# Kernel optimization log

Hardware: AMD Instinct MI355X
Metric: run time of the kernel (lower is better)

## Reference

```python
import jax, jax.numpy as jnp
import numpy as np

B, S, D = 8, 512, 512
H, DK = 64, 8          # 64 heads hardcoded in SelfAttentiveLBLBiLM
WIDTH = 16             # local window width
NL = 2                 # highway layers
N = S + 2 * WIDTH      # padded sequence length


def setup_inputs() -> dict:
    key = jax.random.key(0)
    ks = jax.random.split(key, 12)
    s = 0.02
    return {
        "inputs": jax.random.normal(ks[0], (B, S, D), jnp.float32),
        "left_pad": jax.random.normal(ks[1], (WIDTH, D), jnp.float32) * s,
        "right_pad": jax.random.normal(ks[2], (WIDTH, D), jnp.float32) * s,
        "l_Wqkv": jax.random.normal(ks[3], (3, D, D), jnp.float32) * s,
        "l_bqkv": jnp.zeros((3, D), jnp.float32),
        "l_Wo": jax.random.normal(ks[4], (D, D), jnp.float32) * s,
        "l_bo": jnp.zeros((D,), jnp.float32),
        "r_Wqkv": jax.random.normal(ks[5], (3, D, D), jnp.float32) * s,
        "r_bqkv": jnp.zeros((3, D), jnp.float32),
        "r_Wo": jax.random.normal(ks[6], (D, D), jnp.float32) * s,
        "r_bo": jnp.zeros((D,), jnp.float32),
        "lhw_W": jax.random.normal(ks[7], (NL, 2 * D, D), jnp.float32) * s,
        "lhw_b": jnp.zeros((NL, 2 * D), jnp.float32),
        "rhw_W": jax.random.normal(ks[8], (NL, 2 * D, D), jnp.float32) * s,
        "rhw_b": jnp.zeros((NL, 2 * D), jnp.float32),
    }


def _masks(n, width):
    i = jnp.arange(n)[:, None]
    j = jnp.arange(n)[None, :]
    # local_mask: triu(k=-width-1) * (1 - triu(k=1)) -> i-width-1 <= j <= i
    left = (j <= i) & (j >= i - width - 1)
    # right mask is the full flip of the left mask
    right = (j >= i) & (j <= i + width + 1)
    return left, right


def _mha(x, Wqkv, bqkv, Wo, bo, mask):
    b, n, d = x.shape
    # torch Linear: y = x @ W.T + b, W is [out, in]
    qkv = jnp.einsum("bnd,tod->tbno", x, Wqkv) + bqkv[:, None, None, :]
    q, k, v = [t.reshape(b, n, H, DK).transpose(0, 2, 1, 3) for t in qkv]
    scores = jnp.einsum("bhqd,bhkd->bhqk", q, k) / jnp.sqrt(jnp.float32(DK))
    scores = jnp.where(mask[None, None], scores, jnp.float32(-1e9))
    p = jax.nn.softmax(scores, axis=-1)
    out = jnp.einsum("bhqk,bhkd->bhqd", p, v)
    out = out.transpose(0, 2, 1, 3).reshape(b, n, d)
    return out @ Wo.T + bo


def _highway(x, Ws, bs):
    for l in range(NL):
        proj = x @ Ws[l].T + bs[l]
        nonlin = jax.nn.relu(proj[..., :D])
        gate = jax.nn.sigmoid(proj[..., D:])
        x = gate * x + (1.0 - gate) * nonlin
    return x


def reference(inputs, left_pad, right_pad, l_Wqkv, l_bqkv, l_Wo, l_bo,
              r_Wqkv, r_bqkv, r_Wo, r_bo, lhw_W, lhw_b, rhw_W, rhw_b):
    b = inputs.shape[0]
    new_inputs = jnp.concatenate(
        [jnp.broadcast_to(left_pad[None], (b, WIDTH, D)), inputs,
         jnp.broadcast_to(right_pad[None], (b, WIDTH, D))], axis=1)  # [B, N, D]
    left_mask, right_mask = _masks(N, WIDTH)
    new_left = _mha(new_inputs, l_Wqkv, l_bqkv, l_Wo, l_bo, left_mask)
    new_right = _mha(new_inputs, r_Wqkv, r_bqkv, r_Wo, r_bo, right_mask)
    # per-step loop indexes position start + width -> slice [WIDTH : WIDTH + S]
    left_out = _highway(new_left[:, WIDTH:WIDTH + S], lhw_W, lhw_b)
    right_out = _highway(new_right[:, WIDTH:WIDTH + S], rhw_W, rhw_b)
    last = jnp.concatenate([left_out, right_out], axis=-1)  # [B, S, 2D]
    all_layers = last[None]  # [1, B, S, 2D] (single layer stacked on dim 0)
    return (all_layers, last)
```

## Files before the change

### kernel.cpp

```cpp
#include <hip/hip_runtime.h>
#include <math.h>

#define B_ 8
#define S_ 512
#define D_ 512
#define WIDTH_ 16
#define NSEQ 544
#define MROWS 4352
#define MOUT 4096
#define OUTHALF 4194304

typedef _Float16 half8 __attribute__((ext_vector_type(8)));
typedef _Float16 half4 __attribute__((ext_vector_type(4)));
typedef _Float16 half2_t __attribute__((ext_vector_type(2)));
typedef float floatx4 __attribute__((ext_vector_type(4)));

#if defined(__has_builtin)
#if __has_builtin(__builtin_amdgcn_fdot2)
#define HAS_FDOT2 1
#endif
#endif

#define GLD16(g, l) __builtin_amdgcn_global_load_lds(                          \
    (const __attribute__((address_space(1))) void*)(g),                        \
    (__attribute__((address_space(3))) void*)(l), 16, 0, 0)

#define WAIT_VM(n)  asm volatile("s_waitcnt vmcnt(" #n ")" ::: "memory")
#define WAIT_LGKM0() asm volatile("s_waitcnt lgkmcnt(0)" ::: "memory")
#define BARRIER()                                                              \
    do {                                                                       \
        __builtin_amdgcn_s_barrier();                                          \
        asm volatile("" ::: "memory");                                         \
    } while (0)

__device__ __forceinline__ float sigmoidf_(float x) {
    return 1.f / (1.f + __expf(-x));
}

__global__ __launch_bounds__(256)
void gemm_qkv(const _Float16* __restrict__ A,
              const _Float16* __restrict__ B0, const _Float16* __restrict__ B1,
              const float* __restrict__ bias0, const float* __restrict__ bias1,
              _Float16* __restrict__ C16) {
    const int lda = 512, ldb = 512, ldc = 1536;
    __shared__ _Float16 As[2][128 * 32];
    __shared__ _Float16 Bs[2][128 * 32];
    const int t    = threadIdx.x;
    const int wave = t >> 6;
    const int lane = t & 63;
    const int bm = blockIdx.y * 128;
    const int bn = blockIdx.x * 128;
    const int z  = blockIdx.z;
    const _Float16* B = z ? B1 : B0;
    const float* bias = z ? bias1 : bias0;
    _Float16* C = C16 + (size_t)z * MROWS * 1536;
    const int wm = (wave & 1) * 64;
    const int wn = (wave >> 1) * 64;

    const int inst = wave * 2;
    const int r0 = inst * 16 + (lane >> 2);
    const int kf = (lane & 3) * 8;

    const _Float16* Ag0 = A + (size_t)(bm + r0) * lda + kf;
    const _Float16* Ag1 = Ag0 + (size_t)16 * lda;
    const _Float16* Bg0 = B + (size_t)(bn + r0) * ldb + kf;
    const _Float16* Bg1 = Bg0 + (size_t)16 * ldb;
    const int so = inst * 512;

    const int fr = lane & 15;
    const int fq = (lane >> 4) * 8;

    floatx4 acc[4][4] = {};

#define QKV_STAGE(bf_, koff_)                                                  \
    do {                                                                       \
        GLD16(Ag0 + (koff_), &As[bf_][so]);                                    \
        GLD16(Ag1 + (koff_), &As[bf_][so + 512]);                              \
        GLD16(Bg0 + (koff_), &Bs[bf_][so]);                                    \
        GLD16(Bg1 + (koff_), &Bs[bf_][so + 512]);                              \
    } while (0)

    QKV_STAGE(0, 0);
    QKV_STAGE(1, 32);

#pragma unroll
    for (int tt = 0; tt < 16; tt++) {
        const int c = tt & 1;
        if (tt == 15) WAIT_VM(0);
        else          WAIT_VM(4);
        BARRIER();
        half8 af[4], bf[4];
#pragma unroll
        for (int s = 0; s < 4; s++) {
            af[s] = *(const half8*)&As[c][(wm + s * 16 + fr) * 32 + fq];
            bf[s] = *(const half8*)&Bs[c][(wn + s * 16 + fr) * 32 + fq];
        }
        WAIT_LGKM0();
        BARRIER();
        if (tt + 2 < 16) QKV_STAGE(c, (tt + 2) * 32);
#pragma unroll
        for (int i = 0; i < 4; i++)
#pragma unroll
            for (int j = 0; j < 4; j++)
                acc[i][j] = __builtin_amdgcn_mfma_f32_16x16x32_f16(
                    af[i], bf[j], acc[i][j], 0, 0, 0);
    }
#undef QKV_STAGE

    const int rq = (lane >> 4) * 4;
    const int cc = lane & 15;
#pragma unroll
    for (int i = 0; i < 4; i++) {
        const int rbase = bm + wm + i * 16 + rq;
#pragma unroll
        for (int j = 0; j < 4; j++) {
            const int col = bn + wn + j * 16 + cc;
            const float bv = bias[col];
#pragma unroll
            for (int r = 0; r < 4; r++)
                C[(size_t)(rbase + r) * ldc + col] = (_Float16)(acc[i][j][r] + bv);
        }
    }
}

__global__ __launch_bounds__(256)
void gemm_wo(const _Float16* __restrict__ Aall,
             const _Float16* __restrict__ B0, const _Float16* __restrict__ B1,
             const float* __restrict__ bias0, const float* __restrict__ bias1,
             _Float16* __restrict__ x16base) {
    const int lda = 512, ldb = 512;
    __shared__ _Float16 As[2][64 * 32];
    __shared__ _Float16 Bs[2][128 * 32];
    const int t    = threadIdx.x;
    const int wave = t >> 6;
    const int lane = t & 63;
    const int bm = blockIdx.y * 64;
    const int bn = blockIdx.x * 128;
    const int z  = blockIdx.z;
    const _Float16* A = Aall + (size_t)z * MROWS * 512;
    const _Float16* B = z ? B1 : B0;
    const float* bias = z ? bias1 : bias0;
    _Float16* x16 = x16base + (size_t)z * MOUT * 512;

    const int wm = (wave & 1) * 32;
    const int wn = (wave >> 1) * 64;

    const int rA = wave * 16 + (lane >> 2);
    const int rB = wave * 32 + (lane >> 2);
    const int kf = (lane & 3) * 8;

    const _Float16* Ag0 = A + (size_t)(bm + rA) * lda + kf;
    const _Float16* Bg0 = B + (size_t)(bn + rB) * ldb + kf;
    const _Float16* Bg1 = Bg0 + (size_t)16 * ldb;
    const int soA = wave * 512;
    const int soB = wave * 1024;

    const int fr = lane & 15;
    const int fq = (lane >> 4) * 8;

    floatx4 acc[2][4] = {};

#define WO_STAGE(bf_, koff_)                                                   \
    do {                                                                       \
        GLD16(Ag0 + (koff_), &As[bf_][soA]);                                   \
        GLD16(Bg0 + (koff_), &Bs[bf_][soB]);                                   \
        GLD16(Bg1 + (koff_), &Bs[bf_][soB + 512]);                             \
    } while (0)

    WO_STAGE(0, 0);
    WO_STAGE(1, 32);

#pragma unroll
    for (int tt = 0; tt < 16; tt++) {
        const int c = tt & 1;
        if (tt == 15) WAIT_VM(0);
        else          WAIT_VM(3);
        BARRIER();
        half8 af[2], bf[4];
#pragma unroll
        for (int s = 0; s < 2; s++)
            af[s] = *(const half8*)&As[c][(wm + s * 16 + fr) * 32 + fq];
#pragma unroll
        for (int s = 0; s < 4; s++)
            bf[s] = *(const half8*)&Bs[c][(wn + s * 16 + fr) * 32 + fq];
        WAIT_LGKM0();
        BARRIER();
        if (tt + 2 < 16) WO_STAGE(c, (tt + 2) * 32);
#pragma unroll
        for (int i = 0; i < 2; i++)
#pragma unroll
            for (int j = 0; j < 4; j++)
                acc[i][j] = __builtin_amdgcn_mfma_f32_16x16x32_f16(
                    af[i], bf[j], acc[i][j], 0, 0, 0);
    }
#undef WO_STAGE

    const int rq = (lane >> 4) * 4;
    const int cc = lane & 15;
#pragma unroll
    for (int i = 0; i < 2; i++) {
        const int rbase = bm + wm + i * 16 + rq;
#pragma unroll
        for (int r = 0; r < 4; r++) {
            const int row = rbase + r;
            const int b = row / NSEQ;
            const int s = row - b * NSEQ;
            if (s < WIDTH_ || s >= WIDTH_ + S_) continue;
            const int m = b * S_ + s - WIDTH_;
#pragma unroll
            for (int j = 0; j < 4; j++) {
                const int col = bn + wn + j * 16 + cc;
                x16[(size_t)m * 512 + col] = (_Float16)(acc[i][j][r] + bias[col]);
            }
        }
    }
}

__global__ __launch_bounds__(256)
void gemm_hw(const _Float16* __restrict__ x16inbase,
             const _Float16* __restrict__ W0, const _Float16* __restrict__ W1,
             const float* __restrict__ b0, const float* __restrict__ b1,
             _Float16* __restrict__ x16outbase,
             float* __restrict__ outlastbase,
             float* __restrict__ outallbase) {
    const int lda = 512, ldb = 512;
    __shared__ _Float16 As[2][128 * 32];
    __shared__ _Float16 Bn[2][64 * 32];
    __shared__ _Float16 Bg[2][64 * 32];
    const int t    = threadIdx.x;
    const int wave = t >> 6;
    const int lane = t & 63;
    const int bm = blockIdx.y * 128;
    const int bn = blockIdx.x * 64;
    const int z  = blockIdx.z;
    const _Float16* A = x16inbase + (size_t)z * MOUT * 512;
    const _Float16* W = z ? W1 : W0;
    const float* bias = z ? b1 : b0;
    _Float16* x16out = x16outbase ? x16outbase + (size_t)z * MOUT * 512 : nullptr;

    const int wm = (wave & 1) * 64;
    const int wn = (wave >> 1) * 32;

    const int rA = wave * 32 + (lane >> 2);
    const int rB = wave * 16 + (lane >> 2);
    const int kf = (lane & 3) * 8;

    const _Float16* Ag0 = A + (size_t)(bm + rA) * lda + kf;
    const _Float16* Ag1 = Ag0 + (size_t)16 * lda;
    const _Float16* Bn0 = W + (size_t)(bn + rB) * ldb + kf;
    const _Float16* Bg0 = W + (size_t)(512 + bn + rB) * ldb + kf;
    const int soA = wave * 1024;
    const int soB = wave * 512;

    const int fr = lane & 15;
    const int fq = (lane >> 4) * 8;

    floatx4 accn[4][2] = {};
    floatx4 accg[4][2] = {};

#define HW_STAGE(bf_, koff_)                                                   \
    do {                                                                       \
        GLD16(Ag0 + (koff_), &As[bf_][soA]);                                   \
        GLD16(Ag1 + (koff_), &As[bf_][soA + 512]);                             \
        GLD16(Bn0 + (koff_), &Bn[bf_][soB]);                                   \
        GLD16(Bg0 + (koff_), &Bg[bf_][soB]);                                   \
    } while (0)

    HW_STAGE(0, 0);
    HW_STAGE(1, 32);

#pragma unroll
    for (int tt = 0; tt < 16; tt++) {
        const int c = tt & 1;
        if (tt == 15) WAIT_VM(0);
        else          WAIT_VM(4);
        BARRIER();
        half8 af[4], bnf[2], bgf[2];
#pragma unroll
        for (int s = 0; s < 4; s++)
            af[s] = *(const half8*)&As[c][(wm + s * 16 + fr) * 32 + fq];
#pragma unroll
        for (int s = 0; s < 2; s++) {
            bnf[s] = *(const half8*)&Bn[c][(wn + s * 16 + fr) * 32 + fq];
            bgf[s] = *(const half8*)&Bg[c][(wn + s * 16 + fr) * 32 + fq];
        }
        WAIT_LGKM0();
        BARRIER();
        if (tt + 2 < 16) HW_STAGE(c, (tt + 2) * 32);
#pragma unroll
        for (int i = 0; i < 4; i++)
#pragma unroll
            for (int j = 0; j < 2; j++) {
                accn[i][j] = __builtin_amdgcn_mfma_f32_16x16x32_f16(
                    af[i], bnf[j], accn[i][j], 0, 0, 0);
                accg[i][j] = __builtin_amdgcn_mfma_f32_16x16x32_f16(
                    af[i], bgf[j], accg[i][j], 0, 0, 0);
            }
    }
#undef HW_STAGE

    float* outlast = outlastbase ? outlastbase + z * 512 : nullptr;
    float* outall  = outallbase  ? outallbase  + z * 512 : nullptr;

    const int rq = (lane >> 4) * 4;
    const int cc = lane & 15;
#pragma unroll
    for (int i = 0; i < 4; i++) {
        const int rbase = bm + wm + i * 16 + rq;
#pragma unroll
        for (int j = 0; j < 2; j++) {
            const int col = bn + wn + j * 16 + cc;
            const float bnl = bias[col];
            const float bgt = bias[512 + col];
#pragma unroll
            for (int r = 0; r < 4; r++) {
                const int row = rbase + r;
                const float nl = fmaxf(accn[i][j][r] + bnl, 0.f);
                const float g  = sigmoidf_(accg[i][j][r] + bgt);
                const float xo = (float)A[(size_t)row * 512 + col];
                const float v  = g * xo + (1.f - g) * nl;
                if (x16out) {
                    x16out[(size_t)row * 512 + col] = (_Float16)v;
                } else {
                    outlast[(size_t)row * 1024 + col] = v;
                    outall[(size_t)row * 1024 + col] = v;
                }
            }
        }
    }
}

__global__ __launch_bounds__(256)
void attn_win(const _Float16* __restrict__ qkvall, _Float16* __restrict__ attall) {
    const int dir = blockIdx.y;
    const int dlo = dir ? 0 : -(WIDTH_ + 1);
    const _Float16* qkv = qkvall + (size_t)dir * MROWS * 1536;
    _Float16* att = attall + (size_t)dir * MROWS * 512;
    const int tid = blockIdx.x * 256 + threadIdx.x;
    const int h  = tid & 63;
    const int bi = tid >> 6;
    const int i  = bi % NSEQ;
    const int b  = bi / NSEQ;
    const int j0 = i + dlo;
    const float scale = 0.35355339059327373f;

    const half8 q8 = *(const half8*)(qkv + (size_t)bi * 1536 + h * 8);
#if !defined(HAS_FDOT2)
    float q[8];
#pragma unroll
    for (int d = 0; d < 8; d++) q[d] = (float)q8[d];
#endif

    float s[18];
    float mx = -1e30f;
#pragma unroll
    for (int jj = 0; jj < 18; jj++) {
        const int j = j0 + jj;
        const int jc = j < 0 ? 0 : (j > NSEQ - 1 ? NSEQ - 1 : j);
        const half8 k8 = *(const half8*)(qkv + (size_t)(b * NSEQ + jc) * 1536 + 512 + h * 8);
        float d = 0.f;
#if defined(HAS_FDOT2)
#pragma unroll
        for (int p = 0; p < 4; p++) {
            half2_t qa = { q8[2 * p], q8[2 * p + 1] };
            half2_t ka = { k8[2 * p], k8[2 * p + 1] };
            d = __builtin_amdgcn_fdot2(qa, ka, d, false);
        }
#else
#pragma unroll
        for (int dd = 0; dd < 8; dd++) d = fmaf(q[dd], (float)k8[dd], d);
#endif
        s[jj] = (j == jc) ? d * scale : -1e30f;
        mx = fmaxf(mx, s[jj]);
    }
    float sum = 0.f;
#pragma unroll
    for (int jj = 0; jj < 18; jj++) { s[jj] = __expf(s[jj] - mx); sum += s[jj]; }
    const float inv = 1.f / sum;

    float o[8] = {};
#pragma unroll
    for (int jj = 0; jj < 18; jj++) {
        const int j = j0 + jj;
        const int jc = j < 0 ? 0 : (j > NSEQ - 1 ? NSEQ - 1 : j);
        const half8 v8 = *(const half8*)(qkv + (size_t)(b * NSEQ + jc) * 1536 + 1024 + h * 8);
        const float p = s[jj];
#pragma unroll
        for (int dd = 0; dd < 8; dd++) o[dd] = fmaf(p, (float)v8[dd], o[dd]);
    }
    half8 o16;
#pragma unroll
    for (int d = 0; d < 8; d++) o16[d] = (_Float16)(o[d] * inv);
    *(half8*)&att[(size_t)bi * 512 + h * 8] = o16;
}

__global__ void prep(const float* __restrict__ lq, const float* __restrict__ rq,
                     const float* __restrict__ lo, const float* __restrict__ ro,
                     const float* __restrict__ lh, const float* __restrict__ rh,
                     _Float16* __restrict__ wdst,
                     const float* __restrict__ inp,
                     const float* __restrict__ lp,
                     const float* __restrict__ rp,
                     _Float16* __restrict__ padX) {
    const int gb = blockIdx.x;
    if (gb < 4096) {
        int idx = gb * 256 + threadIdx.x;
        const float* src; int off;
        if      (idx < 196608) { src = lq; off = idx; }
        else if (idx < 393216) { src = rq; off = idx - 196608; }
        else if (idx < 458752) { src = lo; off = idx - 393216; }
        else if (idx < 524288) { src = ro; off = idx - 458752; }
        else if (idx < 786432) { src = lh; off = idx - 524288; }
        else                   { src = rh; off = idx - 786432; }
        const float4 v = ((const float4*)src)[off];
        half4 h = { (_Float16)v.x, (_Float16)v.y, (_Float16)v.z, (_Float16)v.w };
        ((half4*)wdst)[idx] = h;
    } else {
        int idx = (gb - 4096) * 256 + threadIdx.x;
        const int c4 = idx & 127;
        const int t  = idx >> 7;
        const int n = t % NSEQ;
        const int b = t / NSEQ;
        const float* src;
        if (n < WIDTH_)            src = lp + n * 512;
        else if (n < WIDTH_ + S_)  src = inp + ((size_t)(b * S_ + n - WIDTH_)) * 512;
        else                       src = rp + (n - WIDTH_ - S_) * 512;
        const float4 v = *(const float4*)(src + c4 * 4);
        half4 h = { (_Float16)v.x, (_Float16)v.y, (_Float16)v.z, (_Float16)v.w };
        *(half4*)&padX[(size_t)t * 512 + c4 * 4] = h;
    }
}

extern "C" void kernel_launch(void* const* d_in, const int* in_sizes, int n_in,
                              void* d_out, int out_size, void* d_ws, size_t ws_size,
                              hipStream_t stream) {
    const float* inputs    = (const float*)d_in[0];
    const float* left_pad  = (const float*)d_in[1];
    const float* right_pad = (const float*)d_in[2];
    const float* l_Wqkv = (const float*)d_in[3];
    const float* l_bqkv = (const float*)d_in[4];
    const float* l_Wo   = (const float*)d_in[5];
    const float* l_bo   = (const float*)d_in[6];
    const float* r_Wqkv = (const float*)d_in[7];
    const float* r_bqkv = (const float*)d_in[8];
    const float* r_Wo   = (const float*)d_in[9];
    const float* r_bo   = (const float*)d_in[10];
    const float* lhw_W  = (const float*)d_in[11];
    const float* lhw_b  = (const float*)d_in[12];
    const float* rhw_W  = (const float*)d_in[13];
    const float* rhw_b  = (const float*)d_in[14];

    float* out = (float*)d_out;
    _Float16* h = (_Float16*)d_ws;

    _Float16* padX16 = h;
    _Float16* w16    = h + 2228224;
    _Float16* lqkv16 = w16;
    _Float16* rqkv16 = w16 + 786432;
    _Float16* lWo16  = w16 + 1572864;
    _Float16* rWo16  = w16 + 1835008;
    _Float16* lhw16  = w16 + 2097152;
    _Float16* rhw16  = w16 + 3145728;
    _Float16* qkv16  = h + 6422528;
    _Float16* att16  = h + 19791872;
    _Float16* x16a   = h + 24248320;
    _Float16* x16b   = h + 28442624;

    float* out_all  = out;
    float* out_last = out + OUTHALF;

    prep<<<6272, 256, 0, stream>>>(l_Wqkv, r_Wqkv, l_Wo, r_Wo, lhw_W, rhw_W, w16,
                                   inputs, left_pad, right_pad, padX16);

    gemm_qkv<<<dim3(12, 34, 2), 256, 0, stream>>>(
        padX16, lqkv16, rqkv16, l_bqkv, r_bqkv, qkv16);

    attn_win<<<dim3(MROWS * 64 / 256, 2), 256, 0, stream>>>(qkv16, att16);

    gemm_wo<<<dim3(4, 68, 2), 256, 0, stream>>>(
        att16, lWo16, rWo16, l_bo, r_bo, x16a);

    gemm_hw<<<dim3(8, 32, 2), 256, 0, stream>>>(
        x16a, lhw16, rhw16, lhw_b, rhw_b, x16b, nullptr, nullptr);
    gemm_hw<<<dim3(8, 32, 2), 256, 0, stream>>>(
        x16b, lhw16 + 524288, rhw16 + 524288, lhw_b + 1024, rhw_b + 1024,
        nullptr, out_last, out_all);
}
```

Measured before the change: 217.2 us.

## Add XCD block swizzle, LDS-staged epilogues, and multi-query attention reuse

Adds an XCD-aware block index remap to the three GEMMs so neighbouring tiles land on the same L2. The QKV and first highway GEMM epilogues now go through LDS and write 16-byte coalesced rows instead of scattered 2-byte stores. The windowed attention kernel has each thread handle 4 consecutive queries, loading each K/V row once and sharing it across them. It also drops the max-subtraction in the softmax, which risks overflow with large scores and changes launch parallelism to 544 blocks.

After: 185.4 us (median of 2 runs). -14.6%, faster.

```diff
diff --git a/kernel.cpp b/kernel.cpp
--- a/kernel.cpp
+++ b/kernel.cpp
@@ -12,14 +12,7 @@
 
 typedef _Float16 half8 __attribute__((ext_vector_type(8)));
 typedef _Float16 half4 __attribute__((ext_vector_type(4)));
-typedef _Float16 half2_t __attribute__((ext_vector_type(2)));
 typedef float floatx4 __attribute__((ext_vector_type(4)));
-
-#if defined(__has_builtin)
-#if __has_builtin(__builtin_amdgcn_fdot2)
-#define HAS_FDOT2 1
-#endif
-#endif
 
 #define GLD16(g, l) __builtin_amdgcn_global_load_lds(                          \
     (const __attribute__((address_space(1))) void*)(g),                        \
@@ -37,20 +30,32 @@
     return 1.f / (1.f + __expf(-x));
 }
 
+__device__ __forceinline__ void xcd_swz(const int nx, const int ny,
+                                        int& bx, int& by, int& bz) {
+    const int flat = blockIdx.x + nx * (blockIdx.y + ny * blockIdx.z);
+    const int nwg  = nx * ny * 2;
+    const int t2   = (flat & 7) * (nwg >> 3) + (flat >> 3);
+    bz = t2 / (nx * ny);
+    const int rem = t2 - bz * nx * ny;
+    by = rem / nx;
+    bx = rem - by * nx;
+}
+
 __global__ __launch_bounds__(256)
 void gemm_qkv(const _Float16* __restrict__ A,
               const _Float16* __restrict__ B0, const _Float16* __restrict__ B1,
               const float* __restrict__ bias0, const float* __restrict__ bias1,
               _Float16* __restrict__ C16) {
     const int lda = 512, ldb = 512, ldc = 1536;
-    __shared__ _Float16 As[2][128 * 32];
-    __shared__ _Float16 Bs[2][128 * 32];
+    __shared__ _Float16 SH[16384];
+    int bx, by, bz;
+    xcd_swz(12, 34, bx, by, bz);
     const int t    = threadIdx.x;
     const int wave = t >> 6;
     const int lane = t & 63;
-    const int bm = blockIdx.y * 128;
-    const int bn = blockIdx.x * 128;
-    const int z  = blockIdx.z;
+    const int bm = by * 128;
+    const int bn = bx * 128;
+    const int z  = bz;
     const _Float16* B = z ? B1 : B0;
     const float* bias = z ? bias1 : bias0;
     _Float16* C = C16 + (size_t)z * MROWS * 1536;
@@ -74,10 +79,10 @@
 
 #define QKV_STAGE(bf_, koff_)                                                  \
     do {                                                                       \
-        GLD16(Ag0 + (koff_), &As[bf_][so]);                                    \
-        GLD16(Ag1 + (koff_), &As[bf_][so + 512]);                              \
-        GLD16(Bg0 + (koff_), &Bs[bf_][so]);                                    \
-        GLD16(Bg1 + (koff_), &Bs[bf_][so + 512]);                              \
+        GLD16(Ag0 + (koff_), &SH[(bf_) * 4096 + so]);                          \
+        GLD16(Ag1 + (koff_), &SH[(bf_) * 4096 + so + 512]);                    \
+        GLD16(Bg0 + (koff_), &SH[8192 + (bf_) * 4096 + so]);                   \
+        GLD16(Bg1 + (koff_), &SH[8192 + (bf_) * 4096 + so + 512]);             \
     } while (0)
 
     QKV_STAGE(0, 0);
@@ -92,8 +97,8 @@
         half8 af[4], bf[4];
 #pragma unroll
         for (int s = 0; s < 4; s++) {
-            af[s] = *(const half8*)&As[c][(wm + s * 16 + fr) * 32 + fq];
-            bf[s] = *(const half8*)&Bs[c][(wn + s * 16 + fr) * 32 + fq];
+            af[s] = *(const half8*)&SH[c * 4096 + (wm + s * 16 + fr) * 32 + fq];
+            bf[s] = *(const half8*)&SH[8192 + c * 4096 + (wn + s * 16 + fr) * 32 + fq];
         }
         WAIT_LGKM0();
         BARRIER();
@@ -111,15 +116,25 @@
     const int cc = lane & 15;
 #pragma unroll
     for (int i = 0; i < 4; i++) {
-        const int rbase = bm + wm + i * 16 + rq;
 #pragma unroll
         for (int j = 0; j < 4; j++) {
-            const int col = bn + wn + j * 16 + cc;
-            const float bv = bias[col];
+            const int col = wn + j * 16 + cc;
+            const float bv = bias[bn + col];
 #pragma unroll
             for (int r = 0; r < 4; r++)
-                C[(size_t)(rbase + r) * ldc + col] = (_Float16)(acc[i][j][r] + bv);
-        }
+                SH[(wm + i * 16 + rq + r) * 128 + col] =
+                    (_Float16)(acc[i][j][r] + bv);
+        }
+    }
+    WAIT_LGKM0();
+    BARRIER();
+#pragma unroll
+    for (int it = 0; it < 8; it++) {
+        const int flat = it * 256 + t;
+        const int row = flat >> 4;
+        const int ch  = flat & 15;
+        *(half8*)&C[(size_t)(bm + row) * ldc + bn + ch * 8] =
+            *(const half8*)&SH[row * 128 + ch * 8];
     }
 }
 
@@ -131,12 +146,14 @@
     const int lda = 512, ldb = 512;
     __shared__ _Float16 As[2][64 * 32];
     __shared__ _Float16 Bs[2][128 * 32];
+    int bx, by, bz;
+    xcd_swz(4, 68, bx, by, bz);
     const int t    = threadIdx.x;
     const int wave = t >> 6;
     const int lane = t & 63;
-    const int bm = blockIdx.y * 64;
-    const int bn = blockIdx.x * 128;
-    const int z  = blockIdx.z;
+    const int bm = by * 64;
+    const int bn = bx * 128;
+    const int z  = bz;
     const _Float16* A = Aall + (size_t)z * MROWS * 512;
     const _Float16* B = z ? B1 : B0;
     const float* bias = z ? bias1 : bias0;
@@ -224,15 +241,17 @@
              float* __restrict__ outlastbase,
              float* __restrict__ outallbase) {
     const int lda = 512, ldb = 512;
-    __shared__ _Float16 As[2][128 * 32];
+    __shared__ _Float16 SA[8192];
     __shared__ _Float16 Bn[2][64 * 32];
     __shared__ _Float16 Bg[2][64 * 32];
+    int bx, by, bz;
+    xcd_swz(8, 32, bx, by, bz);
     const int t    = threadIdx.x;
     const int wave = t >> 6;
     const int lane = t & 63;
-    const int bm = blockIdx.y * 128;
-    const int bn = blockIdx.x * 64;
-    const int z  = blockIdx.z;
+    const int bm = by * 128;
+    const int bn = bx * 64;
+    const int z  = bz;
     const _Float16* A = x16inbase + (size_t)z * MOUT * 512;
     const _Float16* W = z ? W1 : W0;
     const float* bias = z ? b1 : b0;
@@ -260,8 +279,8 @@
 
 #define HW_STAGE(bf_, koff_)                                                   \
     do {                                                                       \
-        GLD16(Ag0 + (koff_), &As[bf_][soA]);                                   \
-        GLD16(Ag1 + (koff_), &As[bf_][soA + 512]);                             \
+        GLD16(Ag0 + (koff_), &SA[(bf_) * 4096 + soA]);                         \
+        GLD16(Ag1 + (koff_), &SA[(bf_) * 4096 + soA + 512]);                   \
         GLD16(Bn0 + (koff_), &Bn[bf_][soB]);                                   \
         GLD16(Bg0 + (koff_), &Bg[bf_][soB]);                                   \
     } while (0)
@@ -278,7 +297,7 @@
         half8 af[4], bnf[2], bgf[2];
 #pragma unroll
         for (int s = 0; s < 4; s++)
-            af[s] = *(const half8*)&As[c][(wm + s * 16 + fr) * 32 + fq];
+            af[s] = *(const half8*)&SA[c * 4096 + (wm + s * 16 + fr) * 32 + fq];
 #pragma unroll
         for (int s = 0; s < 2; s++) {
             bnf[s] = *(const half8*)&Bn[c][(wn + s * 16 + fr) * 32 + fq];
@@ -299,29 +318,54 @@
     }
 #undef HW_STAGE
 
-    float* outlast = outlastbase ? outlastbase + z * 512 : nullptr;
-    float* outall  = outallbase  ? outallbase  + z * 512 : nullptr;
-
     const int rq = (lane >> 4) * 4;
     const int cc = lane & 15;
-#pragma unroll
-    for (int i = 0; i < 4; i++) {
-        const int rbase = bm + wm + i * 16 + rq;
-#pragma unroll
-        for (int j = 0; j < 2; j++) {
-            const int col = bn + wn + j * 16 + cc;
-            const float bnl = bias[col];
-            const float bgt = bias[512 + col];
-#pragma unroll
-            for (int r = 0; r < 4; r++) {
-                const int row = rbase + r;
-                const float nl = fmaxf(accn[i][j][r] + bnl, 0.f);
-                const float g  = sigmoidf_(accg[i][j][r] + bgt);
-                const float xo = (float)A[(size_t)row * 512 + col];
-                const float v  = g * xo + (1.f - g) * nl;
-                if (x16out) {
-                    x16out[(size_t)row * 512 + col] = (_Float16)v;
-                } else {
+    if (x16out) {
+#pragma unroll
+        for (int i = 0; i < 4; i++) {
+#pragma unroll
+            for (int j = 0; j < 2; j++) {
+                const int col = wn + j * 16 + cc;
+                const float bnl = bias[bn + col];
+                const float bgt = bias[512 + bn + col];
+#pragma unroll
+                for (int r = 0; r < 4; r++) {
+                    const int row = wm + i * 16 + rq + r;
+                    const float nl = fmaxf(accn[i][j][r] + bnl, 0.f);
+                    const float g  = sigmoidf_(accg[i][j][r] + bgt);
+                    const float xo = (float)A[(size_t)(bm + row) * 512 + bn + col];
+                    SA[row * 64 + col] = (_Float16)(g * xo + (1.f - g) * nl);
+                }
+            }
+        }
+        WAIT_LGKM0();
+        BARRIER();
+#pragma unroll
+        for (int it = 0; it < 4; it++) {
+            const int flat = it * 256 + t;
+            const int row = flat >> 3;
+            const int ch  = flat & 7;
+            *(half8*)&x16out[(size_t)(bm + row) * 512 + bn + ch * 8] =
+                *(const half8*)&SA[row * 64 + ch * 8];
+        }
+    } else {
+        float* outlast = outlastbase + z * 512;
+        float* outall  = outallbase  + z * 512;
+#pragma unroll
+        for (int i = 0; i < 4; i++) {
+            const int rbase = bm + wm + i * 16 + rq;
+#pragma unroll
+            for (int j = 0; j < 2; j++) {
+                const int col = bn + wn + j * 16 + cc;
+                const float bnl = bias[col];
+                const float bgt = bias[512 + col];
+#pragma unroll
+                for (int r = 0; r < 4; r++) {
+                    const int row = rbase + r;
+                    const float nl = fmaxf(accn[i][j][r] + bnl, 0.f);
+                    const float g  = sigmoidf_(accg[i][j][r] + bgt);
+                    const float xo = (float)A[(size_t)row * 512 + col];
+                    const float v  = g * xo + (1.f - g) * nl;
                     outlast[(size_t)row * 1024 + col] = v;
                     outall[(size_t)row * 1024 + col] = v;
                 }
@@ -332,66 +376,64 @@
 
 __global__ __launch_bounds__(256)
 void attn_win(const _Float16* __restrict__ qkvall, _Float16* __restrict__ attall) {
-    const int dir = blockIdx.y;
-    const int dlo = dir ? 0 : -(WIDTH_ + 1);
+    const int sb  = (blockIdx.x & 7) * 68 + (blockIdx.x >> 3);
+    const int wid = threadIdx.x >> 6;
+    const int h   = threadIdx.x & 63;
+    const int wflat = sb * 4 + wid;
+    const int ig  = wflat % 136;
+    const int db  = wflat / 136;
+    const int b   = db & 7;
+    const int dir = db >> 3;
+    const int i0  = ig * 4;
+    const int dlo = dir ? 0 : -17;
     const _Float16* qkv = qkvall + (size_t)dir * MROWS * 1536;
     _Float16* att = attall + (size_t)dir * MROWS * 512;
-    const int tid = blockIdx.x * 256 + threadIdx.x;
-    const int h  = tid & 63;
-    const int bi = tid >> 6;
-    const int i  = bi % NSEQ;
-    const int b  = bi / NSEQ;
-    const int j0 = i + dlo;
+    const size_t rowb = (size_t)b * NSEQ;
     const float scale = 0.35355339059327373f;
 
-    const half8 q8 = *(const half8*)(qkv + (size_t)bi * 1536 + h * 8);
-#if !defined(HAS_FDOT2)
-    float q[8];
-#pragma unroll
-    for (int d = 0; d < 8; d++) q[d] = (float)q8[d];
-#endif
-
-    float s[18];
-    float mx = -1e30f;
-#pragma unroll
-    for (int jj = 0; jj < 18; jj++) {
+    float q[4][8];
+#pragma unroll
+    for (int tq = 0; tq < 4; tq++) {
+        const half8 q8 = *(const half8*)(qkv + (rowb + i0 + tq) * 1536 + h * 8);
+#pragma unroll
+        for (int d = 0; d < 8; d++) q[tq][d] = (float)q8[d];
+    }
+
+    float o[4][8] = {};
+    float sum[4] = {};
+    const int j0 = i0 + dlo;
+
+#pragma unroll
+    for (int jj = 0; jj < 21; jj++) {
         const int j = j0 + jj;
-        const int jc = j < 0 ? 0 : (j > NSEQ - 1 ? NSEQ - 1 : j);
-        const half8 k8 = *(const half8*)(qkv + (size_t)(b * NSEQ + jc) * 1536 + 512 + h * 8);
-        float d = 0.f;
-#if defined(HAS_FDOT2)
-#pragma unroll
-        for (int p = 0; p < 4; p++) {
-            half2_t qa = { q8[2 * p], q8[2 * p + 1] };
-            half2_t ka = { k8[2 * p], k8[2 * p + 1] };
-            d = __builtin_amdgcn_fdot2(qa, ka, d, false);
-        }
-#else
-#pragma unroll
-        for (int dd = 0; dd < 8; dd++) d = fmaf(q[dd], (float)k8[dd], d);
-#endif
-        s[jj] = (j == jc) ? d * scale : -1e30f;
-        mx = fmaxf(mx, s[jj]);
-    }
-    float sum = 0.f;
-#pragma unroll
-    for (int jj = 0; jj < 18; jj++) { s[jj] = __expf(s[jj] - mx); sum += s[jj]; }
-    const float inv = 1.f / sum;
-
-    float o[8] = {};
-#pragma unroll
-    for (int jj = 0; jj < 18; jj++) {
-        const int j = j0 + jj;
-        const int jc = j < 0 ? 0 : (j > NSEQ - 1 ? NSEQ - 1 : j);
-        const half8 v8 = *(const half8*)(qkv + (size_t)(b * NSEQ + jc) * 1536 + 1024 + h * 8);
-        const float p = s[jj];
-#pragma unroll
-        for (int dd = 0; dd < 8; dd++) o[dd] = fmaf(p, (float)v8[dd], o[dd]);
-    }
-    half8 o16;
-#pragma unroll
-    for (int d = 0; d < 8; d++) o16[d] = (_Float16)(o[d] * inv);
-    *(half8*)&att[(size_t)bi * 512 + h * 8] = o16;
+        if (j < 0 || j > NSEQ - 1) continue;
+        const size_t jbase = (rowb + j) * 1536 + h * 8;
+        const half8 k8 = *(const half8*)(qkv + jbase + 512);
+        const half8 v8 = *(const half8*)(qkv + jbase + 1024);
+        float kv[8], vv[8];
+#pragma unroll
+        for (int d = 0; d < 8; d++) { kv[d] = (float)k8[d]; vv[d] = (float)v8[d]; }
+#pragma unroll
+        for (int tq = 0; tq < 4; tq++) {
+            if (jj < tq || jj > tq + 17) continue;
+            float d = 0.f;
+#pragma unroll
+            for (int dd = 0; dd < 8; dd++) d = fmaf(q[tq][dd], kv[dd], d);
+            const float p = __expf(d * scale);
+            sum[tq] += p;
+#pragma unroll
+            for (int dd = 0; dd < 8; dd++) o[tq][dd] = fmaf(p, vv[dd], o[tq][dd]);
+        }
+    }
+
+#pragma unroll
+    for (int tq = 0; tq < 4; tq++) {
+        const float inv = 1.f / sum[tq];
+        half8 o16;
+#pragma unroll
+        for (int d = 0; d < 8; d++) o16[d] = (_Float16)(o[tq][d] * inv);
+        *(half8*)&att[(rowb + i0 + tq) * 512 + h * 8] = o16;
+    }
 }
 
 __global__ void prep(const float* __restrict__ lq, const float* __restrict__ rq,
@@ -475,7 +517,7 @@
     gemm_qkv<<<dim3(12, 34, 2), 256, 0, stream>>>(
         padX16, lqkv16, rqkv16, l_bqkv, r_bqkv, qkv16);
 
-    attn_win<<<dim3(MROWS * 64 / 256, 2), 256, 0, stream>>>(qkv16, att16);
+    attn_win<<<dim3(544), 256, 0, stream>>>(qkv16, att16);
 
     gemm_wo<<<dim3(4, 68, 2), 256, 0, stream>>>(
         att16, lWo16, rWo16, l_bo, r_bo, x16a);
```
